# Performance work log

Hardware: AMD Instinct MI355X
Metric: run time of the kernel (lower is better)

The kernel has to match this reference:

```python
import jax, jax.numpy as jnp
import numpy as np

# pywt 'haar': dec_lo[::-1] = [1/sqrt2, 1/sqrt2], dec_hi[::-1] = [1/sqrt2, -1/sqrt2]
_S = 1.0 / np.sqrt(2.0)
_LO = np.array([_S, _S], dtype=np.float32)
_HI = np.array([_S, -_S], dtype=np.float32)
# torch: w_xy[i, j] = dec_y[i] * dec_x[j]  (unsqueeze(1) -> rows, unsqueeze(0) -> cols)
W_LL = jnp.asarray(np.outer(_LO, _LO))
W_LH = jnp.asarray(np.outer(_HI, _LO))
W_HL = jnp.asarray(np.outer(_LO, _HI))
W_HH = jnp.asarray(np.outer(_HI, _HI))


def setup_inputs() -> dict:
    key = jax.random.key(0)
    x = jax.random.normal(key, (8, 96, 512, 512), dtype=jnp.float32)
    return {"x": x}


def reference(x):
    # Depthwise 2x2 stride-2 cross-correlation == linear combo of the four
    # stride-2 phase slices of x (the fused form of the 4 grouped convs).
    a = x[:, :, 0::2, 0::2]  # (p=0, q=0)
    b = x[:, :, 0::2, 1::2]  # (p=0, q=1)
    c = x[:, :, 1::2, 0::2]  # (p=1, q=0)
    d = x[:, :, 1::2, 1::2]  # (p=1, q=1)

    def subband(w):
        return w[0, 0] * a + w[0, 1] * b + w[1, 0] * c + w[1, 1] * d

    return (subband(W_LL), subband(W_LH), subband(W_HL), subband(W_HH))
```

## Files before the change

### kernel.cpp

```cpp
#include <hip/hip_runtime.h>


#define IN_W   512
#define IN_H   512
#define OUT_W  256
#define OUT_H  256

__global__ __launch_bounds__(256) void dwt2d_haar_kernel(
    const float* __restrict__ x,
    float* __restrict__ out,
    int n_img, int total)
{
    const long long sub = (long long)n_img * OUT_W * OUT_H;
    float* __restrict__ ll = out;
    float* __restrict__ lh = out + sub;
    float* __restrict__ hl = out + 2 * sub;
    float* __restrict__ hh = out + 3 * sub;

    for (int t = blockIdx.x * blockDim.x + threadIdx.x; t < total;
         t += gridDim.x * blockDim.x) {
        const int img = t >> 15;
        const int rem = t & 32767;
        const int oy  = rem >> 7;
        const int ox2 = rem & 127;

        const float* src = x + (long long)img * (IN_W * IN_H)
                             + (long long)(oy * 2) * IN_W + ox2 * 4;
        const float4 r0 = *reinterpret_cast<const float4*>(src);
        const float4 r1 = *reinterpret_cast<const float4*>(src + IN_W);

        float2 vll, vlh, vhl, vhh;
        {
            const float apb = r0.x + r0.y, amb = r0.x - r0.y;
            const float cpd = r1.x + r1.y, cmd = r1.x - r1.y;
            vll.x = 0.5f * (apb + cpd);
            vlh.x = 0.5f * (apb - cpd);
            vhl.x = 0.5f * (amb + cmd);
            vhh.x = 0.5f * (amb - cmd);
        }
        {
            const float apb = r0.z + r0.w, amb = r0.z - r0.w;
            const float cpd = r1.z + r1.w, cmd = r1.z - r1.w;
            vll.y = 0.5f * (apb + cpd);
            vlh.y = 0.5f * (apb - cpd);
            vhl.y = 0.5f * (amb + cmd);
            vhh.y = 0.5f * (amb - cmd);
        }

        const long long o = (long long)img * (OUT_W * OUT_H)
                          + (long long)oy * OUT_W + ox2 * 2;
        *reinterpret_cast<float2*>(ll + o) = vll;
        *reinterpret_cast<float2*>(lh + o) = vlh;
        *reinterpret_cast<float2*>(hl + o) = vhl;
        *reinterpret_cast<float2*>(hh + o) = vhh;
    }
}

extern "C" void kernel_launch(void* const* d_in, const int* in_sizes, int n_in,
                              void* d_out, int out_size, void* d_ws, size_t ws_size,
                              hipStream_t stream) {
    const float* x = (const float*)d_in[0];
    float* out = (float*)d_out;

    const int n_img = in_sizes[0] / (IN_W * IN_H);
    const int total = n_img * (OUT_H * (OUT_W / 2));

    dim3 block(256);
    dim3 grid(4096);
    dwt2d_haar_kernel<<<grid, block, 0, stream>>>(x, out, n_img, total);
}
```

Before: 323.3 us.

## Stage row-pair sums in LDS, widen stores, use nontemporal loads and stores

Each block now handles a 16-input-row tile of one image. It loads the tile with fully contiguous nontemporal float4 loads, does the horizontal sum/difference, and stages the results in shared memory. After a barrier it combines vertical pairs and writes float4 nontemporal stores to the four subbands. This replaces the old grid-stride loop, which issued float2 stores and strided two-row loads. The cost is a __syncthreads, 32KB of LDS per block, and one block per tile, which lowers occupancy and reduces load/store overlap within a block.

```diff
diff --git a/kernel.cpp b/kernel.cpp
--- a/kernel.cpp
+++ b/kernel.cpp
@@ -1,58 +1,67 @@
 #include <hip/hip_runtime.h>
 
 
-#define IN_W   512
-#define IN_H   512
-#define OUT_W  256
-#define OUT_H  256
+#define IN_W       512
+#define OUT_W      256
+#define TILE_IROWS 16
+#define TILE_OROWS 8
+
+typedef float f32x4 __attribute__((ext_vector_type(4)));
+typedef float f32x2 __attribute__((ext_vector_type(2)));
 
 __global__ __launch_bounds__(256) void dwt2d_haar_kernel(
     const float* __restrict__ x,
     float* __restrict__ out,
-    int n_img, int total)
+    int n_img)
 {
-    const long long sub = (long long)n_img * OUT_W * OUT_H;
+    __shared__ float Lh[TILE_IROWS][OUT_W];
+    __shared__ float Hh[TILE_IROWS][OUT_W];
+
+    const int bid  = blockIdx.x;
+    const int img  = bid >> 5;
+    const int tile = bid & 31;
+    const int tid  = threadIdx.x;
+
+    const float* src = x + (long long)img * (IN_W * IN_W)
+                         + (long long)tile * (TILE_IROWS * IN_W);
+
+#pragma unroll
+    for (int k = 0; k < 8; ++k) {
+        const int f  = tid + k * 256;
+        const int r  = f >> 7;
+        const int c4 = f & 127;
+        const f32x4 v = __builtin_nontemporal_load(
+            reinterpret_cast<const f32x4*>(src + (long long)f * 4));
+        f32x2 s, d;
+        s.x = v.x + v.y; d.x = v.x - v.y;
+        s.y = v.z + v.w; d.y = v.z - v.w;
+        *reinterpret_cast<f32x2*>(&Lh[r][c4 * 2]) = s;
+        *reinterpret_cast<f32x2*>(&Hh[r][c4 * 2]) = d;
+    }
+    __syncthreads();
+
+    const long long sub = (long long)n_img * (OUT_W * OUT_W);
     float* __restrict__ ll = out;
     float* __restrict__ lh = out + sub;
     float* __restrict__ hl = out + 2 * sub;
     float* __restrict__ hh = out + 3 * sub;
+    const long long obase = (long long)img * (OUT_W * OUT_W)
+                          + (long long)tile * (TILE_OROWS * OUT_W);
 
-    for (int t = blockIdx.x * blockDim.x + threadIdx.x; t < total;
-         t += gridDim.x * blockDim.x) {
-        const int img = t >> 15;
-        const int rem = t & 32767;
-        const int oy  = rem >> 7;
-        const int ox2 = rem & 127;
-
-        const float* src = x + (long long)img * (IN_W * IN_H)
-                             + (long long)(oy * 2) * IN_W + ox2 * 4;
-        const float4 r0 = *reinterpret_cast<const float4*>(src);
-        const float4 r1 = *reinterpret_cast<const float4*>(src + IN_W);
-
-        float2 vll, vlh, vhl, vhh;
-        {
-            const float apb = r0.x + r0.y, amb = r0.x - r0.y;
-            const float cpd = r1.x + r1.y, cmd = r1.x - r1.y;
-            vll.x = 0.5f * (apb + cpd);
-            vlh.x = 0.5f * (apb - cpd);
-            vhl.x = 0.5f * (amb + cmd);
-            vhh.x = 0.5f * (amb - cmd);
-        }
-        {
-            const float apb = r0.z + r0.w, amb = r0.z - r0.w;
-            const float cpd = r1.z + r1.w, cmd = r1.z - r1.w;
-            vll.y = 0.5f * (apb + cpd);
-            vlh.y = 0.5f * (apb - cpd);
-            vhl.y = 0.5f * (amb + cmd);
-            vhh.y = 0.5f * (amb - cmd);
-        }
-
-        const long long o = (long long)img * (OUT_W * OUT_H)
-                          + (long long)oy * OUT_W + ox2 * 2;
-        *reinterpret_cast<float2*>(ll + o) = vll;
-        *reinterpret_cast<float2*>(lh + o) = vlh;
-        *reinterpret_cast<float2*>(hl + o) = vhl;
-        *reinterpret_cast<float2*>(hh + o) = vhh;
+#pragma unroll
+    for (int k = 0; k < 2; ++k) {
+        const int g    = tid + k * 256;
+        const int orow = g >> 6;
+        const int c4   = g & 63;
+        const f32x4 L0 = *reinterpret_cast<const f32x4*>(&Lh[2 * orow][c4 * 4]);
+        const f32x4 L1 = *reinterpret_cast<const f32x4*>(&Lh[2 * orow + 1][c4 * 4]);
+        const f32x4 H0 = *reinterpret_cast<const f32x4*>(&Hh[2 * orow][c4 * 4]);
+        const f32x4 H1 = *reinterpret_cast<const f32x4*>(&Hh[2 * orow + 1][c4 * 4]);
+        const long long o = obase + (long long)g * 4;
+        __builtin_nontemporal_store(0.5f * (L0 + L1), reinterpret_cast<f32x4*>(ll + o));
+        __builtin_nontemporal_store(0.5f * (L0 - L1), reinterpret_cast<f32x4*>(lh + o));
+        __builtin_nontemporal_store(0.5f * (H0 + H1), reinterpret_cast<f32x4*>(hl + o));
+        __builtin_nontemporal_store(0.5f * (H0 - H1), reinterpret_cast<f32x4*>(hh + o));
     }
 }
 
@@ -62,10 +71,8 @@
     const float* x = (const float*)d_in[0];
     float* out = (float*)d_out;
 
-    const int n_img = in_sizes[0] / (IN_W * IN_H);
-    const int total = n_img * (OUT_H * (OUT_W / 2));
+    const int n_img  = in_sizes[0] / (IN_W * IN_W);
+    const int blocks = n_img * 32;
 
-    dim3 block(256);
-    dim3 grid(4096);
-    dwt2d_haar_kernel<<<grid, block, 0, stream>>>(x, out, n_img, total);
+    dwt2d_haar_kernel<<<dim3(blocks), dim3(256), 0, stream>>>(x, out, n_img);
 }
```

After: 282.3 us, median of 2. -12.7%, faster.
